# Kernel tuning notes

Hardware: AMD Instinct MI355X
Metric: run time of the kernel (lower is better)

Reference implementation:

```python
import jax, jax.numpy as jnp
import numpy as np

# FP4 lookup table (E2M1-style values) exactly as in FP4Codec.FP4_TABLE
FP4_TABLE = jnp.array([0.0, 0.5, 1.0, 1.5, 2.0, 3.0, 4.0, 6.0,
                       0.0, -0.5, -1.0, -1.5, -2.0, -3.0, -4.0, -6.0],
                      dtype=jnp.float32)

M, K, N = 128, 4096, 16384


def setup_inputs() -> dict:
    key = jax.random.key(0)
    k1, k2, k3, k4 = jax.random.split(key, 4)
    x = jax.random.normal(k1, (M, K), dtype=jnp.float32)
    # packed bytes: each int holds two 4-bit FP4 indices (hi<<4 | lo)
    weight_fp4 = jax.random.randint(k2, (N, K // 2), 0, 256, dtype=jnp.int32)
    # positive per-output-channel scale (encode guarantees >= 1e-8)
    weight_scale = jax.random.uniform(k3, (N,), dtype=jnp.float32,
                                      minval=1e-3, maxval=2e-2)
    bias = jax.random.normal(k4, (N,), dtype=jnp.float32) * 0.02
    return {"x": x, "weight_fp4": weight_fp4,
            "weight_scale": weight_scale, "bias": bias}


def _dequantize(weight_fp4, weight_scale):
    p = weight_fp4.astype(jnp.uint8)
    hi = (p >> 4) & 0xF
    lo = p & 0xF
    # interleave [hi, lo] along last dim -> [N, K] indices
    idx = jnp.stack([hi, lo], axis=-1).reshape(p.shape[0], -1)
    return FP4_TABLE[idx] * weight_scale[:, None]  # [N, K] fp32


def reference(x, weight_fp4, weight_scale, bias):
    w = _dequantize(weight_fp4, weight_scale)          # [N, K]
    y = jnp.einsum('mk,nk->mn', x, w) + bias            # [M, N]
    return jax.nn.gelu(y, approximate=False)            # exact GELU like F.gelu
```

## Files before the change

### kernel.cpp

```cpp
#include <hip/hip_runtime.h>
#include <stdint.h>


#define M_DIM 128
#define K_DIM 4096
#define N_DIM 16384
#define BN    64
#define BK    64
#define NK    (K_DIM/BK)
#define NT    512
#define NBLK  (N_DIM/BN)

#define AOFF(b) ((b)*16384)
#define BOFF(b) (65536 + (b)*8192)
#define LDS_SZ  98304

typedef __attribute__((ext_vector_type(8))) __bf16 bf16x8;
typedef __attribute__((ext_vector_type(4))) float  f32x4;
typedef unsigned short ushort_t;

__device__ __forceinline__ unsigned f2b_bits(float f) {
  unsigned u = __builtin_bit_cast(unsigned, f);
  u += 0x7FFFu + ((u >> 16) & 1u);
  return u >> 16;
}

__global__ __launch_bounds__(256) void convert_x_kernel(
    const float* __restrict__ x, ushort_t* __restrict__ xb) {
  int i = (blockIdx.x * blockDim.x + threadIdx.x) * 4;
  float4 v = *(const float4*)(x + i);
  ushort4 p;
  p.x = (ushort_t)f2b_bits(v.x);
  p.y = (ushort_t)f2b_bits(v.y);
  p.z = (ushort_t)f2b_bits(v.z);
  p.w = (ushort_t)f2b_bits(v.w);
  *(ushort4*)(xb + i) = p;
}

__device__ __forceinline__ void gl16(const void* g, void* l) {
  __builtin_amdgcn_global_load_lds(
      (const __attribute__((address_space(1))) void*)g,
      (__attribute__((address_space(3))) void*)l, 16, 0, 0);
}

__device__ __forceinline__ bf16x8 decode8(uint4 p) {
  unsigned u01 = __builtin_amdgcn_perm(p.y, p.x, 0x04000400u);
  unsigned u23 = __builtin_amdgcn_perm(p.w, p.z, 0x04000400u);
  unsigned q   = __builtin_amdgcn_perm(u23, u01, 0x05040100u);
  unsigned e  = (q >> 4) & 0x0F0F0F0Fu;
  unsigned o  = q & 0x0F0F0F0Fu;
  unsigned em = e & 0x07070707u, om = o & 0x07070707u;
  unsigned elo = __builtin_amdgcn_perm(0xC0804000u, 0xC0800000u, em);
  unsigned ehi = __builtin_amdgcn_perm(0x40404040u, 0x3F3F3F00u, em);
  unsigned olo = __builtin_amdgcn_perm(0xC0804000u, 0xC0800000u, om);
  unsigned ohi = __builtin_amdgcn_perm(0x40404040u, 0x3F3F3F00u, om);
  ehi |= (e & 0x08080808u) << 4;
  ohi |= (o & 0x08080808u) << 4;
  unsigned t0 = __builtin_amdgcn_perm(ehi, elo, 0x05010400u);
  unsigned t1 = __builtin_amdgcn_perm(ohi, olo, 0x05010400u);
  unsigned t2 = __builtin_amdgcn_perm(ehi, elo, 0x07030602u);
  unsigned t3 = __builtin_amdgcn_perm(ohi, olo, 0x07030602u);
  uint4 r;
  r.x = __builtin_amdgcn_perm(t1, t0, 0x05040100u);
  r.y = __builtin_amdgcn_perm(t1, t0, 0x07060302u);
  r.z = __builtin_amdgcn_perm(t3, t2, 0x05040100u);
  r.w = __builtin_amdgcn_perm(t3, t2, 0x07060302u);
  return __builtin_bit_cast(bf16x8, r);
}

#define MFMA16(a_, b_, c_) __builtin_amdgcn_mfma_f32_16x16x32_bf16(a_, b_, c_, 0, 0, 0)

__global__ __launch_bounds__(NT) void fp4gemm_kernel(
    const ushort_t* __restrict__ xsrc,
    const int*  __restrict__ wq,
    const float* __restrict__ scale,
    const float* __restrict__ bias,
    float* __restrict__ out) {
  __shared__ __align__(16) uint8_t lds[LDS_SZ];

  const int t   = threadIdx.x;
  const int w   = t >> 6;
  const int l   = t & 63;
  const int l16 = l & 15;
  const int lq  = l >> 4;
  const int mq  = w >> 1;
  const int nh  = w & 1;

  const int bid = blockIdx.x;
  const int n0  = ((bid & 7) * 32 + (bid >> 3)) * BN;

  const int srow = t >> 3;
  const int scol = (t & 7) * 16;
  const int sswz = (srow & 7) << 4;
  const int scbs = scol ^ sswz;
  const int bwr  = srow * 128 + (scol ^ sswz);

  const uint8_t* xb  = (const uint8_t*)xsrc;
  const uint8_t* wqb = (const uint8_t*)wq;

  uint4 rb0, rb1, rb2, rb3, rb4, rb5;

#define ISSUE_A1(k_, b_) do { \
  gl16(xb + (size_t)(srow) * 8192 + (size_t)(k_) * 128 + scbs, \
       lds + AOFF(b_) + w * 1024); \
  gl16(xb + (size_t)(64 + srow) * 8192 + (size_t)(k_) * 128 + scbs, \
       lds + AOFF(b_) + 8192 + w * 1024); \
} while (0)

#define ISSUE_B1(k_, s_) do { \
  rb##s_ = *(const uint4*)(wqb + (size_t)(n0 + srow) * 8192 + \
                           (size_t)(k_) * 128 + scol); \
} while (0)

#define DEC1(s_, b_) do { \
  *(bf16x8*)(lds + BOFF(b_) + bwr) = decode8(rb##s_); \
} while (0)

#define WAITV(N_) asm volatile("s_waitcnt vmcnt(" #N_ ")" ::: "memory")
#define BARRIER() do { \
  asm volatile("s_waitcnt lgkmcnt(0)" ::: "memory"); \
  __builtin_amdgcn_s_barrier(); \
  __builtin_amdgcn_sched_barrier(0); \
} while (0)

  f32x4 acc00 = {0,0,0,0}, acc01 = {0,0,0,0};
  f32x4 acc10 = {0,0,0,0}, acc11 = {0,0,0,0};

  const int aR0 = (mq * 32 + l16) * 128;
  const int bR0 = (nh * 32 + l16) * 128;
  const int cB  = (lq << 4) ^ ((l16 & 7) << 4);

#define COMPUTE(b_) do { \
  const uint8_t* Ab_ = lds + AOFF(b_); \
  const uint8_t* Bb_ = lds + BOFF(b_); \
  _Pragma("unroll") \
  for (int ks_ = 0; ks_ < 2; ++ks_) { \
    const int cS_ = (ks_ << 6) ^ cB; \
    bf16x8 a0_ = *(const bf16x8*)(Ab_ + aR0 + cS_); \
    bf16x8 a1_ = *(const bf16x8*)(Ab_ + aR0 + 2048 + cS_); \
    bf16x8 b0_ = *(const bf16x8*)(Bb_ + bR0 + cS_); \
    bf16x8 b1_ = *(const bf16x8*)(Bb_ + bR0 + 2048 + cS_); \
    acc00 = MFMA16(a0_, b0_, acc00); \
    acc01 = MFMA16(a0_, b1_, acc01); \
    acc10 = MFMA16(a1_, b0_, acc10); \
    acc11 = MFMA16(a1_, b1_, acc11); \
  } \
} while (0)

#define BODY(k_, ca_, cb_, ba_, bb_, sa_, sb_, ia_, ib_, W_) do { \
  WAITV(W_); \
  BARRIER(); \
  DEC1(sa_, ba_); DEC1(sb_, bb_); \
  ISSUE_A1((k_) + 2, ba_); ISSUE_A1((k_) + 3, bb_); \
  ISSUE_B1((k_) + 6, ia_); ISSUE_B1((k_) + 7, ib_); \
  __builtin_amdgcn_s_setprio(1); \
  COMPUTE(ca_); COMPUTE(cb_); \
  __builtin_amdgcn_s_setprio(0); \
} while (0)

#define GROUP6(k0_) do { \
  BODY((k0_)+0,  0,1, 2,3, 2,3, 0,1, 2); \
  BODY((k0_)+2,  2,3, 0,1, 4,5, 2,3, 2); \
  BODY((k0_)+4,  0,1, 2,3, 0,1, 4,5, 2); \
  BODY((k0_)+6,  2,3, 0,1, 2,3, 0,1, 2); \
  BODY((k0_)+8,  0,1, 2,3, 4,5, 2,3, 2); \
  BODY((k0_)+10, 2,3, 0,1, 0,1, 4,5, 2); \
} while (0)

  ISSUE_B1(0, 0); ISSUE_B1(1, 1);
  ISSUE_A1(0, 0); ISSUE_A1(1, 1);
  ISSUE_B1(2, 2); ISSUE_B1(3, 3);
  ISSUE_B1(4, 4); ISSUE_B1(5, 5);
  WAITV(8);
  DEC1(0, 0); DEC1(1, 1);

  for (int j = 0; j < 4; ++j) GROUP6(12 * j);

  BODY(48, 0,1, 2,3, 2,3, 0,1, 2);
  BODY(50, 2,3, 0,1, 4,5, 2,3, 2);
  BODY(52, 0,1, 2,3, 0,1, 4,5, 2);
  BODY(54, 2,3, 0,1, 2,3, 0,1, 2);
  BODY(56, 0,1, 2,3, 4,5, 2,3, 2);
  WAITV(2); BARRIER();
  DEC1(0, 0); DEC1(1, 1);
  ISSUE_A1(60, 0); ISSUE_A1(61, 1);
  __builtin_amdgcn_s_setprio(1); COMPUTE(2); COMPUTE(3);
  __builtin_amdgcn_s_setprio(0);
  WAITV(0); BARRIER();
  DEC1(2, 2); DEC1(3, 3);
  ISSUE_A1(62, 2); ISSUE_A1(63, 3);
  __builtin_amdgcn_s_setprio(1); COMPUTE(0); COMPUTE(1);
  __builtin_amdgcn_s_setprio(0);
  WAITV(0); BARRIER();
  __builtin_amdgcn_s_setprio(1); COMPUTE(2); COMPUTE(3);
  __builtin_amdgcn_s_setprio(0);

#pragma unroll
  for (int c = 0; c < 2; ++c) {
    const int ngc = n0 + nh * 32 + c * 16 + l16;
    const float s  = scale[ngc];
    const float bb = bias[ngc];
    f32x4 v0 = c ? acc01 : acc00;
    f32x4 v1 = c ? acc11 : acc10;
#pragma unroll
    for (int fr = 0; fr < 2; ++fr) {
      f32x4 vv = fr ? v1 : v0;
#pragma unroll
      for (int j = 0; j < 4; ++j) {
        int m = mq * 32 + fr * 16 + lq * 4 + j;
        float y = vv[j] * s + bb;
        float g = 0.5f * y * (1.0f + erff(y * 0.70710678118654752f));
        out[(size_t)m * N_DIM + ngc] = g;
      }
    }
  }
#undef ISSUE_A1
#undef ISSUE_B1
#undef DEC1
#undef WAITV
#undef BARRIER
#undef COMPUTE
#undef BODY
#undef GROUP6
}

__global__ __launch_bounds__(NT) void fp4gemm_fallback_kernel(
    const float* __restrict__ x, const int* __restrict__ wq,
    const float* __restrict__ scale, const float* __restrict__ bias,
    float* __restrict__ out) {
  __shared__ __align__(16) uint8_t lds[49152];
  const int t = threadIdx.x, w = t >> 6, l = t & 63;
  const int l16 = l & 15, lq = l >> 4, mq = w >> 1, nh = w & 1;
  const int n0 = (int)blockIdx.x * 64;
  const int srow = t >> 3, scol = (t & 7) * 16, sswz = (srow & 7) << 4;
  const int bwr = srow * 128 + (scol ^ sswz);
  const uint8_t* wqb = (const uint8_t*)wq;
  f32x4 acc00 = {0,0,0,0}, acc01 = {0,0,0,0};
  f32x4 acc10 = {0,0,0,0}, acc11 = {0,0,0,0};
  const int aR0 = (mq * 32 + l16) * 128;
  const int bR0 = (nh * 32 + l16) * 128;
  const int cB  = (lq << 4) ^ ((l16 & 7) << 4);
  for (int kt = 0; kt < 64; ++kt) {
    __syncthreads();
    int bb = kt & 1;
#pragma unroll
    for (int i = 0; i < 2; ++i) {
      const float* xf = x + (size_t)(i * 64 + srow) * K_DIM + (size_t)kt * 64 + (scol >> 1);
      float4 v0 = *(const float4*)(xf);
      float4 v1 = *(const float4*)(xf + 4);
      uint4 pk = make_uint4(f2b_bits(v0.x) | (f2b_bits(v0.y) << 16),
                            f2b_bits(v0.z) | (f2b_bits(v0.w) << 16),
                            f2b_bits(v1.x) | (f2b_bits(v1.y) << 16),
                            f2b_bits(v1.z) | (f2b_bits(v1.w) << 16));
      *(uint4*)(lds + bb * 16384 + (size_t)(i * 64 + srow) * 128 + (scol ^ sswz)) = pk;
    }
    {
      uint4 pv = *(const uint4*)(wqb + (size_t)(n0 + srow) * 8192 + (size_t)kt * 128 + scol);
      *(bf16x8*)(lds + 32768 + bb * 8192 + bwr) = decode8(pv);
    }
    __syncthreads();
    {
      const uint8_t* Ab_ = lds + bb * 16384;
      const uint8_t* Bb_ = lds + 32768 + bb * 8192;
#pragma unroll
      for (int ks = 0; ks < 2; ++ks) {
        const int cS = (ks << 6) ^ cB;
        bf16x8 a0 = *(const bf16x8*)(Ab_ + aR0 + cS);
        bf16x8 a1 = *(const bf16x8*)(Ab_ + aR0 + 2048 + cS);
        bf16x8 b0 = *(const bf16x8*)(Bb_ + bR0 + cS);
        bf16x8 b1 = *(const bf16x8*)(Bb_ + bR0 + 2048 + cS);
        acc00 = MFMA16(a0, b0, acc00);
        acc01 = MFMA16(a0, b1, acc01);
        acc10 = MFMA16(a1, b0, acc10);
        acc11 = MFMA16(a1, b1, acc11);
      }
    }
  }
#pragma unroll
  for (int c = 0; c < 2; ++c) {
    const int ngc = n0 + nh * 32 + c * 16 + l16;
    const float s = scale[ngc];
    const float bv = bias[ngc];
    f32x4 v0 = c ? acc01 : acc00;
    f32x4 v1 = c ? acc11 : acc10;
#pragma unroll
    for (int fr = 0; fr < 2; ++fr) {
      f32x4 vv = fr ? v1 : v0;
#pragma unroll
      for (int j = 0; j < 4; ++j) {
        int m = mq * 32 + fr * 16 + lq * 4 + j;
        float y = vv[j] * s + bv;
        out[(size_t)m * N_DIM + ngc] =
            0.5f * y * (1.0f + erff(y * 0.70710678118654752f));
      }
    }
  }
}

extern "C" void kernel_launch(void* const* d_in, const int* in_sizes, int n_in,
                              void* d_out, int out_size, void* d_ws, size_t ws_size,
                              hipStream_t stream) {
  const float* x     = (const float*)d_in[0];
  const int*   wq    = (const int*)d_in[1];
  const float* scale = (const float*)d_in[2];
  const float* bias  = (const float*)d_in[3];
  float* out = (float*)d_out;

  const size_t xb_bytes = (size_t)M_DIM * K_DIM * 2;
  if (ws_size >= xb_bytes) {
    ushort_t* xb = (ushort_t*)d_ws;
    convert_x_kernel<<<(M_DIM * K_DIM) / (256 * 4), 256, 0, stream>>>(x, xb);
    fp4gemm_kernel<<<NBLK, NT, 0, stream>>>(xb, wq, scale, bias, out);
  } else {
    fp4gemm_fallback_kernel<<<N_DIM / 64, NT, 0, stream>>>(
        x, wq, scale, bias, out);
  }
}
```

Before: 47.36 us.

## Split M across two blocks per N tile with a single-step 4-buffer pipeline

The grid doubles so that each block computes a 64x64 output tile (one M half) instead of 64x128. Each wave now handles a 32x16 sub-tile with two accumulators. The LDS footprint drops to 64KB, which allows two blocks per CU, and the pipeline becomes a uniform 4-stage ring with one k-tile per barrier. The goal is more resident waves to hide the latency of the weight loads. The cost is that each packed weight tile is fetched and decoded twice, once per M half, which relies on cache hits from the paired blocks.

Result: faster. 42.65 us (-10.0%).

```diff
diff --git a/kernel.cpp b/kernel.cpp
--- a/kernel.cpp
+++ b/kernel.cpp
@@ -5,15 +5,12 @@
 #define M_DIM 128
 #define K_DIM 4096
 #define N_DIM 16384
-#define BN    64
-#define BK    64
-#define NK    (K_DIM/BK)
 #define NT    512
-#define NBLK  (N_DIM/BN)
-
-#define AOFF(b) ((b)*16384)
-#define BOFF(b) (65536 + (b)*8192)
-#define LDS_SZ  98304
+#define NBLK  512
+
+#define ABOFF(b) ((b)*8192)
+#define BBOFF(b) (32768 + (b)*8192)
+#define LDS_SZ   65536
 
 typedef __attribute__((ext_vector_type(8))) __bf16 bf16x8;
 typedef __attribute__((ext_vector_type(4))) float  f32x4;
@@ -70,7 +67,7 @@
 
 #define MFMA16(a_, b_, c_) __builtin_amdgcn_mfma_f32_16x16x32_bf16(a_, b_, c_, 0, 0, 0)
 
-__global__ __launch_bounds__(NT) void fp4gemm_kernel(
+__global__ __launch_bounds__(NT, 4) void fp4gemm_kernel(
     const ushort_t* __restrict__ xsrc,
     const int*  __restrict__ wq,
     const float* __restrict__ scale,
@@ -83,11 +80,12 @@
   const int l   = t & 63;
   const int l16 = l & 15;
   const int lq  = l >> 4;
-  const int mq  = w >> 1;
-  const int nh  = w & 1;
-
-  const int bid = blockIdx.x;
-  const int n0  = ((bid & 7) * 32 + (bid >> 3)) * BN;
+  const int mh2 = w >> 2;
+  const int nq  = w & 3;
+
+  const int bid  = blockIdx.x;
+  const int n0   = ((bid & 7) * 32 + (bid >> 4)) * 64;
+  const int mblk = (bid >> 3) & 1;
 
   const int srow = t >> 3;
   const int scol = (t & 7) * 16;
@@ -97,23 +95,20 @@
 
   const uint8_t* xb  = (const uint8_t*)xsrc;
   const uint8_t* wqb = (const uint8_t*)wq;
-
-  uint4 rb0, rb1, rb2, rb3, rb4, rb5;
-
-#define ISSUE_A1(k_, b_) do { \
-  gl16(xb + (size_t)(srow) * 8192 + (size_t)(k_) * 128 + scbs, \
-       lds + AOFF(b_) + w * 1024); \
-  gl16(xb + (size_t)(64 + srow) * 8192 + (size_t)(k_) * 128 + scbs, \
-       lds + AOFF(b_) + 8192 + w * 1024); \
-} while (0)
+  const size_t aRowBase = (size_t)(mblk * 64 + srow) * 8192;
+
+  uint4 rq0, rq1, rq2, rq3;
+
+#define ISSUE_A1(k_, b_) \
+  gl16(xb + aRowBase + (size_t)(k_) * 128 + scbs, lds + ABOFF(b_) + w * 1024)
 
 #define ISSUE_B1(k_, s_) do { \
-  rb##s_ = *(const uint4*)(wqb + (size_t)(n0 + srow) * 8192 + \
+  rq##s_ = *(const uint4*)(wqb + (size_t)(n0 + srow) * 8192 + \
                            (size_t)(k_) * 128 + scol); \
 } while (0)
 
 #define DEC1(s_, b_) do { \
-  *(bf16x8*)(lds + BOFF(b_) + bwr) = decode8(rb##s_); \
+  *(bf16x8*)(lds + BBOFF(b_) + bwr) = decode8(rq##s_); \
 } while (0)
 
 #define WAITV(N_) asm volatile("s_waitcnt vmcnt(" #N_ ")" ::: "memory")
@@ -123,91 +118,68 @@
   __builtin_amdgcn_sched_barrier(0); \
 } while (0)
 
-  f32x4 acc00 = {0,0,0,0}, acc01 = {0,0,0,0};
-  f32x4 acc10 = {0,0,0,0}, acc11 = {0,0,0,0};
-
-  const int aR0 = (mq * 32 + l16) * 128;
-  const int bR0 = (nh * 32 + l16) * 128;
+  f32x4 acc0 = {0,0,0,0}, acc1 = {0,0,0,0};
+
+  const int aR0 = (mh2 * 32 + l16) * 128;
+  const int bR0 = (nq * 16 + l16) * 128;
   const int cB  = (lq << 4) ^ ((l16 & 7) << 4);
 
 #define COMPUTE(b_) do { \
-  const uint8_t* Ab_ = lds + AOFF(b_); \
-  const uint8_t* Bb_ = lds + BOFF(b_); \
+  const uint8_t* Ab_ = lds + ABOFF(b_); \
+  const uint8_t* Bb_ = lds + BBOFF(b_); \
   _Pragma("unroll") \
   for (int ks_ = 0; ks_ < 2; ++ks_) { \
     const int cS_ = (ks_ << 6) ^ cB; \
+    bf16x8 b0_ = *(const bf16x8*)(Bb_ + bR0 + cS_); \
     bf16x8 a0_ = *(const bf16x8*)(Ab_ + aR0 + cS_); \
     bf16x8 a1_ = *(const bf16x8*)(Ab_ + aR0 + 2048 + cS_); \
-    bf16x8 b0_ = *(const bf16x8*)(Bb_ + bR0 + cS_); \
-    bf16x8 b1_ = *(const bf16x8*)(Bb_ + bR0 + 2048 + cS_); \
-    acc00 = MFMA16(a0_, b0_, acc00); \
-    acc01 = MFMA16(a0_, b1_, acc01); \
-    acc10 = MFMA16(a1_, b0_, acc10); \
-    acc11 = MFMA16(a1_, b1_, acc11); \
+    acc0 = MFMA16(a0_, b0_, acc0); \
+    acc1 = MFMA16(a1_, b0_, acc1); \
   } \
 } while (0)
 
-#define BODY(k_, ca_, cb_, ba_, bb_, sa_, sb_, ia_, ib_, W_) do { \
-  WAITV(W_); \
+#define BODY(k_, u_, c_) do { \
+  WAITV(2); \
   BARRIER(); \
-  DEC1(sa_, ba_); DEC1(sb_, bb_); \
-  ISSUE_A1((k_) + 2, ba_); ISSUE_A1((k_) + 3, bb_); \
-  ISSUE_B1((k_) + 6, ia_); ISSUE_B1((k_) + 7, ib_); \
-  __builtin_amdgcn_s_setprio(1); \
-  COMPUTE(ca_); COMPUTE(cb_); \
-  __builtin_amdgcn_s_setprio(0); \
-} while (0)
-
-#define GROUP6(k0_) do { \
-  BODY((k0_)+0,  0,1, 2,3, 2,3, 0,1, 2); \
-  BODY((k0_)+2,  2,3, 0,1, 4,5, 2,3, 2); \
-  BODY((k0_)+4,  0,1, 2,3, 0,1, 4,5, 2); \
-  BODY((k0_)+6,  2,3, 0,1, 2,3, 0,1, 2); \
-  BODY((k0_)+8,  0,1, 2,3, 4,5, 2,3, 2); \
-  BODY((k0_)+10, 2,3, 0,1, 0,1, 4,5, 2); \
-} while (0)
-
-  ISSUE_B1(0, 0); ISSUE_B1(1, 1);
+  DEC1(u_, u_); \
+  ISSUE_B1((k_) + 6, u_); \
+  ISSUE_A1((k_) + 2, u_); \
+  COMPUTE(c_); \
+} while (0)
+
+  ISSUE_B1(0, 0); ISSUE_B1(1, 1); ISSUE_B1(2, 2); ISSUE_B1(3, 3);
   ISSUE_A1(0, 0); ISSUE_A1(1, 1);
-  ISSUE_B1(2, 2); ISSUE_B1(3, 3);
-  ISSUE_B1(4, 4); ISSUE_B1(5, 5);
-  WAITV(8);
+  WAITV(4);
   DEC1(0, 0); DEC1(1, 1);
-
-  for (int j = 0; j < 4; ++j) GROUP6(12 * j);
-
-  BODY(48, 0,1, 2,3, 2,3, 0,1, 2);
-  BODY(50, 2,3, 0,1, 4,5, 2,3, 2);
-  BODY(52, 0,1, 2,3, 0,1, 4,5, 2);
-  BODY(54, 2,3, 0,1, 2,3, 0,1, 2);
-  BODY(56, 0,1, 2,3, 4,5, 2,3, 2);
-  WAITV(2); BARRIER();
-  DEC1(0, 0); DEC1(1, 1);
-  ISSUE_A1(60, 0); ISSUE_A1(61, 1);
-  __builtin_amdgcn_s_setprio(1); COMPUTE(2); COMPUTE(3);
-  __builtin_amdgcn_s_setprio(0);
-  WAITV(0); BARRIER();
-  DEC1(2, 2); DEC1(3, 3);
-  ISSUE_A1(62, 2); ISSUE_A1(63, 3);
-  __builtin_amdgcn_s_setprio(1); COMPUTE(0); COMPUTE(1);
-  __builtin_amdgcn_s_setprio(0);
-  WAITV(0); BARRIER();
-  __builtin_amdgcn_s_setprio(1); COMPUTE(2); COMPUTE(3);
-  __builtin_amdgcn_s_setprio(0);
-
-#pragma unroll
-  for (int c = 0; c < 2; ++c) {
-    const int ngc = n0 + nh * 32 + c * 16 + l16;
+  ISSUE_B1(4, 0); ISSUE_B1(5, 1);
+  WAITV(3); BARRIER();
+  DEC1(2, 2); ISSUE_B1(6, 2); ISSUE_A1(2, 2); COMPUTE(0);
+  WAITV(4); BARRIER();
+  DEC1(3, 3); ISSUE_B1(7, 3); ISSUE_A1(3, 3); COMPUTE(1);
+  for (int j = 0; j < 14; ++j) {
+    const int kt = 2 + 4 * j;
+    BODY(kt + 0, 0, 2);
+    BODY(kt + 1, 1, 3);
+    BODY(kt + 2, 2, 0);
+    BODY(kt + 3, 3, 1);
+  }
+  WAITV(2); BARRIER(); DEC1(0, 0); ISSUE_A1(60, 0); COMPUTE(2);
+  WAITV(1); BARRIER(); DEC1(1, 1); ISSUE_A1(61, 1); COMPUTE(3);
+  WAITV(1); BARRIER(); DEC1(2, 2); ISSUE_A1(62, 2); COMPUTE(0);
+  WAITV(1); BARRIER(); DEC1(3, 3); ISSUE_A1(63, 3); COMPUTE(1);
+  WAITV(1); BARRIER(); COMPUTE(2);
+  WAITV(0); BARRIER(); COMPUTE(3);
+
+  {
+    const int ngc = n0 + nq * 16 + l16;
     const float s  = scale[ngc];
     const float bb = bias[ngc];
-    f32x4 v0 = c ? acc01 : acc00;
-    f32x4 v1 = c ? acc11 : acc10;
 #pragma unroll
     for (int fr = 0; fr < 2; ++fr) {
-      f32x4 vv = fr ? v1 : v0;
+      f32x4 vv = fr ? acc1 : acc0;
 #pragma unroll
       for (int j = 0; j < 4; ++j) {
-        int m = mq * 32 + fr * 16 + lq * 4 + j;
+        int m = mblk * 64 + mh2 * 32 + fr * 16 + lq * 4 + j;
         float y = vv[j] * s + bb;
         float g = 0.5f * y * (1.0f + erff(y * 0.70710678118654752f));
         out[(size_t)m * N_DIM + ngc] = g;
@@ -221,10 +193,9 @@
 #undef BARRIER
 #undef COMPUTE
 #undef BODY
-#undef GROUP6
-}
-
-__global__ __launch_bounds__(NT) void fp4gemm_fallback_kernel(
+}
+
+__global__ __launch_bounds__(512) void fp4gemm_fallback_kernel(
     const float* __restrict__ x, const int* __restrict__ wq,
     const float* __restrict__ scale, const float* __restrict__ bias,
     float* __restrict__ out) {
@@ -312,7 +283,7 @@
     convert_x_kernel<<<(M_DIM * K_DIM) / (256 * 4), 256, 0, stream>>>(x, xb);
     fp4gemm_kernel<<<NBLK, NT, 0, stream>>>(xb, wq, scale, bias, out);
   } else {
-    fp4gemm_fallback_kernel<<<N_DIM / 64, NT, 0, stream>>>(
+    fp4gemm_fallback_kernel<<<N_DIM / 64, 512, 0, stream>>>(
         x, wq, scale, bias, out);
   }
 }
```
